# Kernel tuning notes

Hardware: AMD Instinct MI355X
Metric: run time of the kernel (lower is better)

The kernel has to match this reference:

```python
import jax, jax.numpy as jnp
import numpy as np
from jax import lax

MAX_DEPTH = 8
NLEAVES = 2 ** MAX_DEPTH      # 256
NNODES = 2 ** MAX_DEPTH - 1   # 255 (preorder-numbered inner nodes)
NCLASS = 10
EPS = 1e-5
BATCH = 8192


def _build_paths():
    # Reproduce the torch preorder node numbering and DFS leaf numbering.
    node_ctr = [0]
    leaf_paths = []
    def rec(depth, path):
        idx = node_ctr[0]; node_ctr[0] += 1
        if depth < MAX_DEPTH:
            rec(depth + 1, path + [(idx, 0)])   # left child: prob (1 - p)
            rec(depth + 1, path + [(idx, 1)])   # right child: prob p
        else:
            leaf_paths.append(path + [(idx, 0)])
            leaf_paths.append(path + [(idx, 1)])
    rec(1, [])
    nidx = np.array([[n for n, _ in p] for p in leaf_paths], dtype=np.int32)  # [L, D]
    dirs = np.array([[d for _, d in p] for p in leaf_paths], dtype=bool)      # [L, D]
    return nidx, dirs

NODE_IDX, DIRS = _build_paths()


def _bn(x, g, b):
    # training-mode batchnorm over all dims except channel axis 1 (biased var)
    axes = tuple(i for i in range(x.ndim) if i != 1)
    m = x.mean(axes, keepdims=True)
    v = x.var(axes, keepdims=True)
    shape = [1] * x.ndim; shape[1] = -1
    return (x - m) * lax.rsqrt(v + EPS) * g.reshape(shape) + b.reshape(shape)


def _conv(x, w, b):
    y = lax.conv_general_dilated(x, w, (1, 1), 'VALID',
                                 dimension_numbers=('NCHW', 'OIHW', 'NCHW'))
    return y + b[None, :, None, None]


def _pool2(x):
    return lax.reduce_window(x, -jnp.inf, lax.max, (1, 1, 2, 2), (1, 1, 2, 2), 'VALID')


def setup_inputs() -> dict:
    ks = jax.random.split(jax.random.key(0), 12)
    f32 = jnp.float32
    return {
        'x': jax.random.normal(ks[0], (BATCH, 1, 28, 28), f32),
        'y': jax.random.randint(ks[1], (BATCH,), 0, NCLASS),
        'conv1_w': 0.1 * jax.random.normal(ks[2], (20, 1, 5, 5), f32),
        'conv1_b': jnp.zeros((20,), f32),
        'conv2_w': 0.05 * jax.random.normal(ks[3], (50, 20, 5, 5), f32),
        'conv2_b': jnp.zeros((50,), f32),
        'g1': jnp.ones((20,), f32), 'be1': jnp.zeros((20,), f32),
        'g2': jnp.ones((50,), f32), 'be2': jnp.zeros((50,), f32),
        'fc1_w': 0.05 * jax.random.normal(ks[4], (10, 800), f32),
        'fc1_b': jnp.zeros((10,), f32),
        'g3': jnp.ones((10,), f32), 'be3': jnp.zeros((10,), f32),
        'theta_w': 0.3 * jax.random.normal(ks[5], (NNODES, 10), f32),
        'theta_b': jnp.zeros((NNODES,), f32),
        'pi': jax.random.uniform(ks[6], (NLEAVES, NCLASS), f32, 0.1, 1.0),
    }


def reference(x, y, conv1_w, conv1_b, conv2_w, conv2_b, g1, be1, g2, be2,
              fc1_w, fc1_b, g3, be3, theta_w, theta_b, pi):
    B = x.shape[0]
    # CNN backbone
    h = _pool2(jax.nn.relu(_bn(_conv(x, conv1_w, conv1_b), g1, be1)))
    h = _pool2(jax.nn.relu(_bn(_conv(h, conv2_w, conv2_b), g2, be2)))
    h = h.reshape(B, 4 * 4 * 50)
    h = jax.nn.relu(_bn(h @ fc1_w.T + fc1_b, g3, be3))        # [B, 10]
    # batched soft-tree gating: one fused GEMM for all 255 tiny Linear(10,1)
    p = jax.nn.sigmoid(h @ theta_w.T + theta_b)                # [B, NNODES]
    g = p[:, NODE_IDX]                                         # [B, L, D]
    mu = jnp.prod(jnp.where(DIRS[None], g, 1.0 - g), axis=2)   # [B, L]
    # pi is a row-stochastic distribution (uniform at torch init)
    pi_n = pi / pi.sum(1, keepdims=True)
    # stale P from __init__: uniform mu (1/L) @ pi  ->  column means of pi
    P_prev = jnp.broadcast_to(pi_n.mean(0), (B, NCLASS))       # [B, C]
    # vectorized cal_pi (soft-EM update of leaf distributions)
    Y = jax.nn.one_hot(y, NCLASS, dtype=mu.dtype)              # [B, C]
    S = mu.T @ (Y / P_prev)                                    # [L, C]
    pi_h = pi_n * S
    pi_new = pi_h / pi_h.sum(1, keepdims=True)
    # cal_P and log
    P = mu @ pi_new                                            # [B, C]
    return jnp.log(P)
```

## Files before the change

kernel.cpp:

```cpp
#include <hip/hip_runtime.h>
#include <hip/hip_bf16.h>
#include <math.h>

typedef __attribute__((ext_vector_type(8))) short short8v;
typedef __attribute__((ext_vector_type(4))) float float4v;

static const size_t F_RAWP1B = 0;
static const size_t F_C2P    = 14155776;
static const size_t F_PART1  = 20709376;
static const size_t F_PART2  = 21037056;
static const size_t F_PART3  = 21241856;
static const size_t F_BN1    = 21246976;
static const size_t F_BN2    = 21247016;
static const size_t F_BN3    = 21247116;
static const size_t F_SRAW   = 21247136;
static const size_t F_PINEW  = 21249696;
static const size_t F_WB2    = 21252256;
static const size_t F_WB1    = 21271712;
static const size_t F_SPART  = 21272224;
static const size_t F_HRAW   = 0;
static const size_t F_MU     = 81920;

__device__ __forceinline__ float relu_(float v) { return v > 0.f ? v : 0.f; }

__device__ __forceinline__ unsigned int pack_bf16x2(float a, float b) {
  __hip_bfloat16 ha = __float2bfloat16(a), hb = __float2bfloat16(b);
  unsigned short ua, ub;
  __builtin_memcpy(&ua, &ha, 2); __builtin_memcpy(&ub, &hb, 2);
  return ((unsigned int)ub << 16) | ua;
}

__device__ __forceinline__ float pick_(float a, float b, bool mx) {
  return mx ? fmaxf(a, b) : fminf(a, b);
}

__global__ __launch_bounds__(256) void k_wprep1(
    const float* __restrict__ w, unsigned short* __restrict__ wb1)
{
  const int i = blockIdx.x * 256 + threadIdx.x;
  const int n = i >> 5, k = i & 31;
  const int kh = k / 6, kw = k - kh*6;
  float v = (n < 20 && kh < 5 && kw < 5) ? w[n*25 + kh*5 + kw] : 0.f;
  __hip_bfloat16 h = __float2bfloat16(v);
  unsigned short u; __builtin_memcpy(&u, &h, 2);
  wb1[i] = u;
}

__global__ __launch_bounds__(256) void k_wprep2(
    const float* __restrict__ w, unsigned short* __restrict__ wb)
{
  const int idx = blockIdx.x * 256 + threadIdx.x;
  const int cc = idx >> 9;
  const int rem = idx & 511;
  const int n = rem >> 3, j = rem & 7;
  float v = 0.f;
  if (cc < 75 && n < 50) {
    const int khw = cc / 3, icg = cc - khw*3;
    const int ic = icg*8 + j;
    if (ic < 20) {
      const int kh = khw / 5, kw = khw - kh*5;
      v = w[((n*20 + ic)*5 + kh)*5 + kw];
    }
  }
  __hip_bfloat16 h = __float2bfloat16(v);
  unsigned short u; __builtin_memcpy(&u, &h, 2);
  wb[idx] = u;
}

__global__ __launch_bounds__(256) void k_conv1_mfma(
    const float* __restrict__ x, const unsigned short* __restrict__ wb1,
    const float* __restrict__ g1, unsigned int* __restrict__ rawp1b,
    float* __restrict__ part)
{
  __shared__ alignas(16) unsigned short xpk[1568];
  __shared__ float sred[4][32], qred[4][32];
  const int tid = threadIdx.x, img = blockIdx.x;
  const float* xp = x + (size_t)img * 784;
  for (int i = tid; i < 784; i += 256) {
    const int r = i / 28, c = i - r*28;
    __hip_bfloat16 h = __float2bfloat16(xp[i]);
    unsigned short u; __builtin_memcpy(&u, &h, 2);
    xpk[r*28 + c] = u;
    if (c >= 1) xpk[784 + r*28 + (c-1)] = u;
    else        xpk[784 + r*28 + 27]  = 0;
  }
  __syncthreads();
  const int wave = tid >> 6, lane = tid & 63, lo = lane & 15, hi = lane >> 4;

  const short8v bfr0 = *(const short8v*)(wb1 + (lo*32 + hi*8));
  const short8v bfr1 = *(const short8v*)(wb1 + ((16+lo)*32 + hi*8));

  const unsigned enc = (hi==0) ? 0x0E020100u
                     : (hi==1) ? 0x1D1C100Fu
                     : (hi==2) ? 0x2C2B2A1Eu
                     :           0x003A3938u;
  const int off0 = enc & 255, off1 = (enc>>8)&255, off2 = (enc>>16)&255, off3 = enc>>24;
  const unsigned int* xpd = (const unsigned int*)xpk;
  const int pb   = (lo & 1) * 392;
  const int oyp  = (lo >> 1) & 1, qoff = lo >> 2;
  const int inv  = pb + (6*wave + oyp)*14;

  float4v acc[9][2];
  #pragma unroll
  for (int t = 0; t < 9; ++t) {
    acc[t][0] = (float4v){0.f,0.f,0.f,0.f};
    acc[t][1] = (float4v){0.f,0.f,0.f,0.f};
  }

  #pragma unroll
  for (int tt = 0; tt < 9; ++tt) {
    const int pylc = (tt*4) / 12;
    const int pxlc = (tt*4) - pylc*12;
    const int base = inv + pylc*28 + pxlc + qoff;
    union { unsigned int u[4]; short8v v; } cu;
    cu.u[0] = xpd[base + off0];
    cu.u[1] = xpd[base + off1];
    cu.u[2] = xpd[base + off2];
    cu.u[3] = xpd[base + off3];
    acc[tt][0] = __builtin_amdgcn_mfma_f32_16x16x32_bf16(cu.v, bfr0, acc[tt][0], 0, 0, 0);
    acc[tt][1] = __builtin_amdgcn_mfma_f32_16x16x32_bf16(cu.v, bfr1, acc[tt][1], 0, 0, 0);
  }

  const bool gp0 = (g1[lo] >= 0.f);
  const bool gp1 = (lo < 4) ? (g1[16+lo] >= 0.f) : true;
  float sv0 = 0.f, qv0 = 0.f, sv1 = 0.f, qv1 = 0.f;
  unsigned int* dst = rawp1b + (size_t)img * 1728;
  #pragma unroll
  for (int tt = 0; tt < 9; ++tt) {
    const int T = wave*9 + tt;
    const int q = T*4 + hi;
    const float4v v0 = acc[tt][0];
    const float4v v1 = acc[tt][1];
    #pragma unroll
    for (int r = 0; r < 4; ++r) { sv0 += v0[r]; qv0 += v0[r]*v0[r]; }
    #pragma unroll
    for (int r = 0; r < 4; ++r) { sv1 += v1[r]; qv1 += v1[r]*v1[r]; }
    const float p0 = pick_(pick_(v0[0], v0[1], gp0), pick_(v0[2], v0[3], gp0), gp0);
    const float p1 = pick_(pick_(v1[0], v1[1], gp1), pick_(v1[2], v1[3], gp1), gp1);
    const float o0 = __shfl_down(p0, 1);
    const float o1 = __shfl_down(p1, 1);
    if ((lo & 1) == 0) {
      dst[q*12 + (lo >> 1)] = pack_bf16x2(p0, o0);
      if (lo < 8)
        dst[q*12 + 8 + (lo >> 1)] = pack_bf16x2(p1, o1);
    }
  }
  sv0 += __shfl_down(sv0, 32); qv0 += __shfl_down(qv0, 32);
  sv0 += __shfl_down(sv0, 16); qv0 += __shfl_down(qv0, 16);
  sv1 += __shfl_down(sv1, 32); qv1 += __shfl_down(qv1, 32);
  sv1 += __shfl_down(sv1, 16); qv1 += __shfl_down(qv1, 16);
  if (hi == 0) {
    sred[wave][lo] = sv0; sred[wave][16+lo] = sv1;
    qred[wave][lo] = qv0; qred[wave][16+lo] = qv1;
  }
  __syncthreads();
  if (tid < 20) {
    float s = 0.f, q = 0.f;
    #pragma unroll
    for (int w2 = 0; w2 < 4; ++w2) { s += sred[w2][tid]; q += qred[w2][tid]; }
    part[(size_t)img*40 + tid]      = s;
    part[(size_t)img*40 + 20 + tid] = q;
  }
}

__global__ __launch_bounds__(256) void k_conv2_mfma(
    const unsigned int* __restrict__ rawp1b, const unsigned short* __restrict__ wb,
    const float* __restrict__ bn1, const float* __restrict__ g2,
    float* __restrict__ c2p, float* __restrict__ part)
{
  __shared__ alignas(16) unsigned int in4[6912];
  __shared__ float sred[4][64], qred[4][64];
  __shared__ alignas(16) float bn1i[48];
  __shared__ unsigned short aofft[76];
  const int tid = threadIdx.x, blk = blockIdx.x;
  if (tid < 24) {
    const float sc = (tid < 20) ? bn1[tid]      : 0.f;
    const float sh = (tid < 20) ? bn1[20 + tid] : 0.f;
    bn1i[2*tid] = sc; bn1i[2*tid + 1] = sh;
  }
  if (tid < 76) {
    const int cc2 = tid > 74 ? 74 : tid;
    const int khw = cc2 / 3, icg = cc2 - khw*3;
    const int kh = khw / 5, kw = khw - kh*5;
    aofft[tid] = (unsigned short)((kh*12 + kw)*48 + icg*16);
  }
  __syncthreads();

  const uint4* src4 = (const uint4*)(rawp1b + (size_t)blk * 6912);
  uint4* dst4 = (uint4*)in4;
  int jj = tid % 3;
  for (int k = 0; k < 7; ++k) {
    const int i = k*256 + tid;
    if (i < 1728) {
      const uint4 v = src4[i];
      unsigned int o[4];
      #pragma unroll
      for (int m = 0; m < 4; ++m) {
        const float4 ss = *(const float4*)(bn1i + jj*16 + m*4);
        const unsigned int u = (m==0) ? v.x : (m==1) ? v.y : (m==2) ? v.z : v.w;
        const float a = __uint_as_float(u << 16);
        const float b = __uint_as_float(u & 0xffff0000u);
        const float ra = relu_(fmaf(a, ss.x, ss.y));
        const float rb = relu_(fmaf(b, ss.z, ss.w));
        o[m] = pack_bf16x2(ra, rb);
      }
      uint4 ov; ov.x = o[0]; ov.y = o[1]; ov.z = o[2]; ov.w = o[3];
      dst4[i] = ov;
    }
    jj = (jj == 2) ? 0 : jj + 1;
  }
  __syncthreads();

  const int wave = tid >> 6, lane = tid & 63;
  const int lo = lane & 15, hi = lane >> 4;
  const char* ibase = (const char*)in4 + wave * 6912;

  const char* bA[4];
  #pragma unroll
  for (int a = 0; a < 4; ++a) {
    const int m = a*16 + lo;
    bA[a] = ibase + ((m >> 3) * 12 + (m & 7)) * 48;
  }
  unsigned short aoffs[19];
  #pragma unroll
  for (int s = 0; s < 19; ++s) aoffs[s] = aofft[s*4 + hi];
  const unsigned short* wbase = wb + hi*512 + lo*8;

  bool gpos[4];
  #pragma unroll
  for (int nf = 0; nf < 4; ++nf) {
    const int n = nf*16 + lo;
    gpos[nf] = (n < 50) ? (g2[n] >= 0.f) : true;
  }

  float4v acc[4][4];
  #pragma unroll
  for (int a = 0; a < 4; ++a)
    #pragma unroll
    for (int nf = 0; nf < 4; ++nf) acc[a][nf] = (float4v){0.f, 0.f, 0.f, 0.f};

  #pragma unroll
  for (int s = 0; s < 19; ++s) {
    short8v av[4], bv[4];
    #pragma unroll
    for (int am = 0; am < 4; ++am)
      av[am] = *(const short8v*)(bA[am] + aoffs[s]);
    const unsigned short* wrow = wbase + s*2048;
    #pragma unroll
    for (int nf = 0; nf < 4; ++nf)
      bv[nf] = *(const short8v*)(wrow + nf*128);
    #pragma unroll
    for (int am = 0; am < 4; ++am)
      #pragma unroll
      for (int nf = 0; nf < 4; ++nf)
        acc[am][nf] = __builtin_amdgcn_mfma_f32_16x16x32_bf16(av[am], bv[nf], acc[am][nf], 0, 0, 0);
  }

  const int img = blk*4 + wave;
  #pragma unroll
  for (int nf = 0; nf < 4; ++nf) {
    const int n = nf*16 + lo;
    float sv = 0.f, qv = 0.f;
    #pragma unroll
    for (int am = 0; am < 4; ++am) {
      float4v v = acc[am][nf];
      #pragma unroll
      for (int r = 0; r < 4; ++r) { sv += v[r]; qv += v[r]*v[r]; }
      float h0 = gpos[nf] ? fmaxf(v[0], v[1]) : fminf(v[0], v[1]);
      float h1 = gpos[nf] ? fmaxf(v[2], v[3]) : fminf(v[2], v[3]);
      const float o0 = __shfl_xor(h0, 32);
      const float o1 = __shfl_xor(h1, 32);
      h0 = gpos[nf] ? fmaxf(h0, o0) : fminf(h0, o0);
      h1 = gpos[nf] ? fmaxf(h1, o1) : fminf(h1, o1);
      if (hi < 2 && n < 50) {
        float2 o; o.x = h0; o.y = h1;
        *(float2*)(c2p + (size_t)img*800 + n*16 + am*4 + hi*2) = o;
      }
    }
    sv += __shfl_down(sv, 32); qv += __shfl_down(qv, 32);
    sv += __shfl_down(sv, 16); qv += __shfl_down(qv, 16);
    if (hi == 0) { sred[wave][nf*16 + lo] = sv; qred[wave][nf*16 + lo] = qv; }
  }
  __syncthreads();
  if (tid < 100) {
    const int ch = tid < 50 ? tid : tid - 50;
    float t = 0.f;
    if (tid < 50) {
      #pragma unroll
      for (int w2 = 0; w2 < 4; ++w2) t += sred[w2][ch];
      part[(size_t)blk*100 + ch] = t;
    } else {
      #pragma unroll
      for (int w2 = 0; w2 < 4; ++w2) t += qred[w2][ch];
      part[(size_t)blk*100 + 50 + ch] = t;
    }
  }
}

__global__ __launch_bounds__(256) void k_bn_fin(
    const float* __restrict__ part, int nblk, int nch, float N,
    const float* __restrict__ g, const float* __restrict__ b,
    float* __restrict__ out)
{
  __shared__ double rd[4][2];
  const int tid = threadIdx.x, ch = blockIdx.x;
  const int lane = tid & 63, wid = tid >> 6;
  double s = 0.0, q = 0.0;
  for (int i = tid; i < nblk; i += 256) {
    s += (double)part[(size_t)i*2*nch + ch];
    q += (double)part[(size_t)i*2*nch + nch + ch];
  }
  #pragma unroll
  for (int off = 32; off > 0; off >>= 1) { s += __shfl_down(s, off); q += __shfl_down(q, off); }
  if (lane == 0) { rd[wid][0] = s; rd[wid][1] = q; }
  __syncthreads();
  if (tid == 0) {
    double S = rd[0][0] + rd[1][0] + rd[2][0] + rd[3][0];
    double Q = rd[0][1] + rd[1][1] + rd[2][1] + rd[3][1];
    double mean = S / (double)N;
    double var  = Q / (double)N - mean * mean;
    if (var < 0.0) var = 0.0;
    float scv = (float)((double)g[ch] / sqrt(var + 1e-5));
    out[ch]       = scv;
    out[nch + ch] = b[ch] - (float)mean * scv;
  }
}

__global__ __launch_bounds__(256) void k_fc1(
    const float* __restrict__ c2p, const float* __restrict__ bn2,
    const float* __restrict__ fw, float* __restrict__ h_raw,
    float* __restrict__ part)
{
  __shared__ alignas(16) float wl[8000];
  __shared__ float s2[50], h2[50];
  __shared__ float red[4][20];
  const int tid = threadIdx.x;
  for (int i = tid; i < 2000; i += 256)
    ((float4*)wl)[i] = ((const float4*)fw)[i];
  if (tid < 50) { s2[tid] = bn2[tid]; h2[tid] = bn2[50 + tid]; }
  __syncthreads();
  const int s = tid >> 3, kc = tid & 7;
  const int sample = blockIdx.x * 32 + s;
  const float* xr = c2p + (size_t)sample * 800 + kc * 100;
  float acc[10];
  #pragma unroll
  for (int f = 0; f < 10; ++f) acc[f] = 0.f;
  #pragma unroll 5
  for (int c = 0; c < 25; ++c) {
    const int k = kc*100 + c*4;
    float4 v = *(const float4*)(xr + c*4);
    const int oc = k >> 4;
    const float sc = s2[oc], sh = h2[oc];
    v.x = relu_(v.x*sc + sh); v.y = relu_(v.y*sc + sh);
    v.z = relu_(v.z*sc + sh); v.w = relu_(v.w*sc + sh);
    #pragma unroll
    for (int f = 0; f < 10; ++f) {
      const float4 wv = *(const float4*)(wl + f*800 + k);
      acc[f] += v.x*wv.x + v.y*wv.y + v.z*wv.z + v.w*wv.w;
    }
  }
  const int lane = tid & 63, wid = tid >> 6;
  #pragma unroll
  for (int f = 0; f < 10; ++f) {
    acc[f] += __shfl_down(acc[f], 4);
    acc[f] += __shfl_down(acc[f], 2);
    acc[f] += __shfl_down(acc[f], 1);
    float a2 = (kc == 0) ? acc[f] : 0.f;
    float q2 = (kc == 0) ? acc[f]*acc[f] : 0.f;
    if (kc == 0) h_raw[(size_t)sample*10 + f] = acc[f];
    a2 += __shfl_down(a2, 32); q2 += __shfl_down(q2, 32);
    a2 += __shfl_down(a2, 16); q2 += __shfl_down(q2, 16);
    a2 += __shfl_down(a2, 8);  q2 += __shfl_down(q2, 8);
    if (lane == 0) { red[wid][f] = a2; red[wid][10+f] = q2; }
  }
  __syncthreads();
  if (tid < 20) {
    float t = 0.f;
    #pragma unroll
    for (int w2 = 0; w2 < 4; ++w2) t += red[w2][tid];
    part[(size_t)blockIdx.x*20 + tid] = t;
  }
}

__global__ __launch_bounds__(256) void k_theta_mu(
    const float* __restrict__ h_raw, const float* __restrict__ bn3,
    const float* __restrict__ tw, const float* __restrict__ tb,
    float* __restrict__ mu)
{
  __shared__ float twt[10][256];
  __shared__ float tbl[256];
  __shared__ float hl[32][10];
  __shared__ float pl[32][256];
  const int tid = threadIdx.x, blk = blockIdx.x;
  for (int i = tid; i < 2550; i += 256) {
    const int node = i / 10, f = i - node*10;
    twt[f][node] = tw[i];
  }
  if (tid < 10) twt[tid][255] = 0.f;
  tbl[tid] = (tid < 255) ? tb[tid] : 0.f;
  for (int i = tid; i < 320; i += 256) {
    const int ss = i / 10, f = i - ss*10;
    hl[ss][f] = relu_(h_raw[(size_t)blk*320 + i] * bn3[f] + bn3[10 + f]);
  }
  __syncthreads();
  const int node = tid;
  for (int i2 = 0; i2 < 32; ++i2) {
    float h[10];
    #pragma unroll
    for (int f = 0; f < 10; ++f) h[f] = hl[i2][f];
    float d = tbl[node];
    #pragma unroll
    for (int f = 0; f < 10; ++f) d += h[f] * twt[f][node];
    pl[i2][node] = (node < 255) ? 1.f / (1.f + __expf(-d)) : 0.f;
  }
  __syncthreads();
  for (int i2 = 0; i2 < 32; ++i2) {
    float m = 1.f; int idx = 0;
    #pragma unroll
    for (int k = 0; k < 8; ++k) {
      const int dir = (tid >> (7 - k)) & 1;
      const float pv = pl[i2][idx];
      m *= dir ? pv : (1.f - pv);
      idx += dir ? (1 << (7 - k)) : 1;
    }
    mu[(size_t)(blk*32 + i2)*256 + tid] = m;
  }
}

__global__ __launch_bounds__(256) void k_S_part(
    const float* __restrict__ mu, const int* __restrict__ y,
    float* __restrict__ spart)
{
  const int tid = threadIdx.x;
  const int b0 = blockIdx.x * 32;
  float acc[10];
  #pragma unroll
  for (int c = 0; c < 10; ++c) acc[c] = 0.f;
  for (int s = 0; s < 32; ++s) {
    const int b = b0 + s;
    const float m = mu[(size_t)b*256 + tid];
    const int c = y[b];
    #pragma unroll
    for (int cc = 0; cc < 10; ++cc) acc[cc] += (c == cc) ? m : 0.f;
  }
  float* dst = spart + (size_t)blockIdx.x*2560 + tid*10;
  #pragma unroll
  for (int cc = 0; cc < 10; ++cc) dst[cc] = acc[cc];
}

__global__ __launch_bounds__(256) void k_S_red(
    const float* __restrict__ spart, float* __restrict__ S)
{
  const int e = blockIdx.x * 256 + threadIdx.x;
  float s = 0.f;
  for (int k = 0; k < 256; ++k) s += spart[(size_t)k*2560 + e];
  S[e] = s;
}

__global__ __launch_bounds__(256) void k_pi(
    const float* __restrict__ pi, const float* __restrict__ S,
    float* __restrict__ pi_new)
{
  __shared__ float pin[2560];
  __shared__ float Pp[10];
  const int t = threadIdx.x;
  float row[10]; float rs = 0.f;
  #pragma unroll
  for (int c = 0; c < 10; ++c) { row[c] = pi[t*10 + c]; rs += row[c]; }
  #pragma unroll
  for (int c = 0; c < 10; ++c) { row[c] /= rs; pin[t*10 + c] = row[c]; }
  __syncthreads();
  if (t < 10) {
    float s = 0.f;
    for (int l = 0; l < 256; ++l) s += pin[l*10 + t];
    Pp[t] = s / 256.f;
  }
  __syncthreads();
  float hs = 0.f; float ph[10];
  #pragma unroll
  for (int c = 0; c < 10; ++c) {
    const float Sv = S[t*10 + c] / Pp[c];
    ph[c] = row[c] * Sv;
    hs += ph[c];
  }
  #pragma unroll
  for (int c = 0; c < 10; ++c) pi_new[t*10 + c] = ph[c] / hs;
}

__global__ __launch_bounds__(256) void k_out(
    const float* __restrict__ mu, const float* __restrict__ pn,
    float* __restrict__ out)
{
  __shared__ float plt[10][260];
  const int tid = threadIdx.x;
  if (tid < 256) {
    #pragma unroll
    for (int c = 0; c < 10; ++c) plt[c][tid] = pn[tid*10 + c];
  }
  __syncthreads();
  const int gid = blockIdx.x * 256 + tid;
  const int b = gid / 10, c = gid % 10;
  const float4* mr4 = (const float4*)(mu + (size_t)b * 256);
  const float*  pc  = &plt[c][0];
  float a0 = 0.f, a1 = 0.f;
  #pragma unroll 4
  for (int l4 = 0; l4 < 64; ++l4) {
    const float4 m = mr4[l4];
    const float4 p = *(const float4*)(pc + 4*l4);
    a0 += m.x*p.x + m.y*p.y;
    a1 += m.z*p.z + m.w*p.w;
  }
  out[gid] = logf(a0 + a1);
}

extern "C" void kernel_launch(void* const* d_in, const int* in_sizes, int n_in,
                              void* d_out, int out_size, void* d_ws, size_t ws_size,
                              hipStream_t stream)
{
  const float* x   = (const float*)d_in[0];
  const int*   y   = (const int*)  d_in[1];
  const float* c1w = (const float*)d_in[2];
  const float* c2w = (const float*)d_in[4];
  const float* g1  = (const float*)d_in[6];
  const float* be1 = (const float*)d_in[7];
  const float* g2  = (const float*)d_in[8];
  const float* be2 = (const float*)d_in[9];
  const float* fw  = (const float*)d_in[10];
  const float* g3  = (const float*)d_in[12];
  const float* be3 = (const float*)d_in[13];
  const float* thw = (const float*)d_in[14];
  const float* thb = (const float*)d_in[15];
  const float* pi  = (const float*)d_in[16];
  float* ws  = (float*)d_ws;
  float* out = (float*)d_out;

  unsigned int*   rawp1b = (unsigned int*)(ws + F_RAWP1B);
  float*          c2p    = ws + F_C2P;
  float*          part1  = ws + F_PART1;
  float*          part2  = ws + F_PART2;
  float*          part3  = ws + F_PART3;
  float*          bn1    = ws + F_BN1;
  float*          bn2    = ws + F_BN2;
  float*          bn3    = ws + F_BN3;
  float*          sraw   = ws + F_SRAW;
  float*          pinew  = ws + F_PINEW;
  unsigned short* wb2    = (unsigned short*)(ws + F_WB2);
  unsigned short* wb1    = (unsigned short*)(ws + F_WB1);
  float*          spart  = ws + F_SPART;
  float*          hraw   = ws + F_HRAW;
  float*          muB    = ws + F_MU;

  k_wprep1<<<4, 256, 0, stream>>>(c1w, wb1);
  k_wprep2<<<152, 256, 0, stream>>>(c2w, wb2);
  k_conv1_mfma<<<8192, 256, 0, stream>>>(x, wb1, g1, rawp1b, part1);
  k_bn_fin<<<20, 256, 0, stream>>>(part1, 8192, 20, 8192.f * 576.f, g1, be1, bn1);
  k_conv2_mfma<<<2048, 256, 0, stream>>>(rawp1b, wb2, bn1, g2, c2p, part2);
  k_bn_fin<<<50, 256, 0, stream>>>(part2, 2048, 50, 8192.f * 64.f, g2, be2, bn2);
  k_fc1<<<256, 256, 0, stream>>>(c2p, bn2, fw, hraw, part3);
  k_bn_fin<<<10, 256, 0, stream>>>(part3, 256, 10, 8192.f, g3, be3, bn3);
  k_theta_mu<<<256, 256, 0, stream>>>(hraw, bn3, thw, thb, muB);
  k_S_part<<<256, 256, 0, stream>>>(muB, y, spart);
  k_S_red<<<10, 256, 0, stream>>>(spart, sraw);
  k_pi<<<1, 256, 0, stream>>>(pi, sraw, pinew);
  k_out<<<320, 256, 0, stream>>>(muB, pinew, out);
}
```

Baseline: 187.4 us.

## Process multiple images per block with register-staged prefetch in conv1 and conv2

conv1 now handles four images per block and conv2 two image groups per block. In both, the next image's global load goes into registers while the current one is computed on MFMA, with double-buffered LDS in conv1. This hides global load latency behind MFMA work and amortises the per-block weight and setup loads. The cost is a quarter and a half as many blocks, extra register pressure from the staging buffers (which may lower occupancy), and an added barrier per iteration.

```diff
diff --git a/kernel.cpp b/kernel.cpp
--- a/kernel.cpp
+++ b/kernel.cpp
@@ -30,6 +30,12 @@
   return ((unsigned int)ub << 16) | ua;
 }
 
+__device__ __forceinline__ unsigned short cvt_bf16(float a) {
+  __hip_bfloat16 h = __float2bfloat16(a);
+  unsigned short u; __builtin_memcpy(&u, &h, 2);
+  return u;
+}
+
 __device__ __forceinline__ float pick_(float a, float b, bool mx) {
   return mx ? fmaxf(a, b) : fminf(a, b);
 }
@@ -41,9 +47,7 @@
   const int n = i >> 5, k = i & 31;
   const int kh = k / 6, kw = k - kh*6;
   float v = (n < 20 && kh < 5 && kw < 5) ? w[n*25 + kh*5 + kw] : 0.f;
-  __hip_bfloat16 h = __float2bfloat16(v);
-  unsigned short u; __builtin_memcpy(&u, &h, 2);
-  wb1[i] = u;
+  wb1[i] = cvt_bf16(v);
 }
 
 __global__ __launch_bounds__(256) void k_wprep2(
@@ -62,9 +66,7 @@
       v = w[((n*20 + ic)*5 + kh)*5 + kw];
     }
   }
-  __hip_bfloat16 h = __float2bfloat16(v);
-  unsigned short u; __builtin_memcpy(&u, &h, 2);
-  wb[idx] = u;
+  wb[idx] = cvt_bf16(v);
 }
 
 __global__ __launch_bounds__(256) void k_conv1_mfma(
@@ -72,94 +74,134 @@
     const float* __restrict__ g1, unsigned int* __restrict__ rawp1b,
     float* __restrict__ part)
 {
-  __shared__ alignas(16) unsigned short xpk[1568];
+  __shared__ alignas(16) unsigned short xpk[2][1568];
   __shared__ float sred[4][32], qred[4][32];
-  const int tid = threadIdx.x, img = blockIdx.x;
-  const float* xp = x + (size_t)img * 784;
-  for (int i = tid; i < 784; i += 256) {
-    const int r = i / 28, c = i - r*28;
-    __hip_bfloat16 h = __float2bfloat16(xp[i]);
-    unsigned short u; __builtin_memcpy(&u, &h, 2);
-    xpk[r*28 + c] = u;
-    if (c >= 1) xpk[784 + r*28 + (c-1)] = u;
-    else        xpk[784 + r*28 + 27]  = 0;
-  }
-  __syncthreads();
+  const int tid = threadIdx.x, blk = blockIdx.x;
+  const int img0 = blk * 4;
   const int wave = tid >> 6, lane = tid & 63, lo = lane & 15, hi = lane >> 4;
 
   const short8v bfr0 = *(const short8v*)(wb1 + (lo*32 + hi*8));
   const short8v bfr1 = *(const short8v*)(wb1 + ((16+lo)*32 + hi*8));
-
   const unsigned enc = (hi==0) ? 0x0E020100u
                      : (hi==1) ? 0x1D1C100Fu
                      : (hi==2) ? 0x2C2B2A1Eu
                      :           0x003A3938u;
   const int off0 = enc & 255, off1 = (enc>>8)&255, off2 = (enc>>16)&255, off3 = enc>>24;
-  const unsigned int* xpd = (const unsigned int*)xpk;
   const int pb   = (lo & 1) * 392;
   const int oyp  = (lo >> 1) & 1, qoff = lo >> 2;
   const int inv  = pb + (6*wave + oyp)*14;
-
-  float4v acc[9][2];
-  #pragma unroll
-  for (int t = 0; t < 9; ++t) {
-    acc[t][0] = (float4v){0.f,0.f,0.f,0.f};
-    acc[t][1] = (float4v){0.f,0.f,0.f,0.f};
-  }
-
-  #pragma unroll
-  for (int tt = 0; tt < 9; ++tt) {
-    const int pylc = (tt*4) / 12;
-    const int pxlc = (tt*4) - pylc*12;
-    const int base = inv + pylc*28 + pxlc + qoff;
-    union { unsigned int u[4]; short8v v; } cu;
-    cu.u[0] = xpd[base + off0];
-    cu.u[1] = xpd[base + off1];
-    cu.u[2] = xpd[base + off2];
-    cu.u[3] = xpd[base + off3];
-    acc[tt][0] = __builtin_amdgcn_mfma_f32_16x16x32_bf16(cu.v, bfr0, acc[tt][0], 0, 0, 0);
-    acc[tt][1] = __builtin_amdgcn_mfma_f32_16x16x32_bf16(cu.v, bfr1, acc[tt][1], 0, 0, 0);
-  }
-
   const bool gp0 = (g1[lo] >= 0.f);
   const bool gp1 = (lo < 4) ? (g1[16+lo] >= 0.f) : true;
-  float sv0 = 0.f, qv0 = 0.f, sv1 = 0.f, qv1 = 0.f;
-  unsigned int* dst = rawp1b + (size_t)img * 1728;
-  #pragma unroll
-  for (int tt = 0; tt < 9; ++tt) {
-    const int T = wave*9 + tt;
-    const int q = T*4 + hi;
-    const float4v v0 = acc[tt][0];
-    const float4v v1 = acc[tt][1];
-    #pragma unroll
-    for (int r = 0; r < 4; ++r) { sv0 += v0[r]; qv0 += v0[r]*v0[r]; }
-    #pragma unroll
-    for (int r = 0; r < 4; ++r) { sv1 += v1[r]; qv1 += v1[r]*v1[r]; }
-    const float p0 = pick_(pick_(v0[0], v0[1], gp0), pick_(v0[2], v0[3], gp0), gp0);
-    const float p1 = pick_(pick_(v1[0], v1[1], gp1), pick_(v1[2], v1[3], gp1), gp1);
-    const float o0 = __shfl_down(p0, 1);
-    const float o1 = __shfl_down(p1, 1);
-    if ((lo & 1) == 0) {
-      dst[q*12 + (lo >> 1)] = pack_bf16x2(p0, o0);
-      if (lo < 8)
-        dst[q*12 + 8 + (lo >> 1)] = pack_bf16x2(p1, o1);
-    }
-  }
-  sv0 += __shfl_down(sv0, 32); qv0 += __shfl_down(qv0, 32);
-  sv0 += __shfl_down(sv0, 16); qv0 += __shfl_down(qv0, 16);
-  sv1 += __shfl_down(sv1, 32); qv1 += __shfl_down(qv1, 32);
-  sv1 += __shfl_down(sv1, 16); qv1 += __shfl_down(qv1, 16);
-  if (hi == 0) {
-    sred[wave][lo] = sv0; sred[wave][16+lo] = sv1;
-    qred[wave][lo] = qv0; qred[wave][16+lo] = qv1;
-  }
-  __syncthreads();
-  if (tid < 20) {
-    float s = 0.f, q = 0.f;
-    #pragma unroll
-    for (int w2 = 0; w2 < 4; ++w2) { s += sred[w2][tid]; q += qred[w2][tid]; }
-    part[(size_t)img*40 + tid]      = s;
-    part[(size_t)img*40 + 20 + tid] = q;
+  const int r0 = tid / 28,        c0 = tid - r0*28;
+  const int r1 = (tid+256) / 28,  c1 = (tid+256) - r1*28;
+  const int r2 = (tid+512) / 28,  c2 = (tid+512) - r2*28;
+  const int r3 = (tid+768) / 28,  c3 = (tid+768) - r3*28;
+
+  float st0, st1, st2, st3;
+  {
+    const float* xp = x + (size_t)img0 * 784;
+    st0 = xp[tid]; st1 = xp[tid+256]; st2 = xp[tid+512];
+    st3 = (tid < 16) ? xp[tid+768] : 0.f;
+  }
+  {
+    unsigned short* b0 = &xpk[0][0];
+    const unsigned short u0 = cvt_bf16(st0), u1 = cvt_bf16(st1), u2 = cvt_bf16(st2);
+    b0[r0*28 + c0] = u0;
+    if (c0 >= 1) b0[784 + r0*28 + c0 - 1] = u0; else b0[784 + r0*28 + 27] = 0;
+    b0[r1*28 + c1] = u1;
+    if (c1 >= 1) b0[784 + r1*28 + c1 - 1] = u1; else b0[784 + r1*28 + 27] = 0;
+    b0[r2*28 + c2] = u2;
+    if (c2 >= 1) b0[784 + r2*28 + c2 - 1] = u2; else b0[784 + r2*28 + 27] = 0;
+    if (tid < 16) {
+      const unsigned short u3 = cvt_bf16(st3);
+      b0[r3*28 + c3] = u3;
+      if (c3 >= 1) b0[784 + r3*28 + c3 - 1] = u3;
+    }
+  }
+  __syncthreads();
+
+  int cur = 0;
+  for (int ii = 0; ii < 4; ++ii) {
+    if (ii < 3) {
+      const float* xp = x + (size_t)(img0 + ii + 1) * 784;
+      st0 = xp[tid]; st1 = xp[tid+256]; st2 = xp[tid+512];
+      st3 = (tid < 16) ? xp[tid+768] : 0.f;
+    }
+    const unsigned int* xpd = (const unsigned int*)&xpk[cur][0];
+    float4v acc[9][2];
+    #pragma unroll
+    for (int t = 0; t < 9; ++t) {
+      acc[t][0] = (float4v){0.f,0.f,0.f,0.f};
+      acc[t][1] = (float4v){0.f,0.f,0.f,0.f};
+    }
+    #pragma unroll
+    for (int tt = 0; tt < 9; ++tt) {
+      const int pylc = (tt*4) / 12;
+      const int pxlc = (tt*4) - pylc*12;
+      const int base = inv + pylc*28 + pxlc + qoff;
+      union { unsigned int u[4]; short8v v; } cu;
+      cu.u[0] = xpd[base + off0];
+      cu.u[1] = xpd[base + off1];
+      cu.u[2] = xpd[base + off2];
+      cu.u[3] = xpd[base + off3];
+      acc[tt][0] = __builtin_amdgcn_mfma_f32_16x16x32_bf16(cu.v, bfr0, acc[tt][0], 0, 0, 0);
+      acc[tt][1] = __builtin_amdgcn_mfma_f32_16x16x32_bf16(cu.v, bfr1, acc[tt][1], 0, 0, 0);
+    }
+    float sv0 = 0.f, qv0 = 0.f, sv1 = 0.f, qv1 = 0.f;
+    unsigned int* dst = rawp1b + (size_t)(img0 + ii) * 1728;
+    #pragma unroll
+    for (int tt = 0; tt < 9; ++tt) {
+      const int T = wave*9 + tt;
+      const int q = T*4 + hi;
+      const float4v v0 = acc[tt][0];
+      const float4v v1 = acc[tt][1];
+      #pragma unroll
+      for (int r = 0; r < 4; ++r) { sv0 += v0[r]; qv0 += v0[r]*v0[r]; }
+      #pragma unroll
+      for (int r = 0; r < 4; ++r) { sv1 += v1[r]; qv1 += v1[r]*v1[r]; }
+      const float p0 = pick_(pick_(v0[0], v0[1], gp0), pick_(v0[2], v0[3], gp0), gp0);
+      const float p1 = pick_(pick_(v1[0], v1[1], gp1), pick_(v1[2], v1[3], gp1), gp1);
+      const float o0 = __shfl_down(p0, 1);
+      const float o1 = __shfl_down(p1, 1);
+      if ((lo & 1) == 0) {
+        dst[q*12 + (lo >> 1)] = pack_bf16x2(p0, o0);
+        if (lo < 8)
+          dst[q*12 + 8 + (lo >> 1)] = pack_bf16x2(p1, o1);
+      }
+    }
+    sv0 += __shfl_down(sv0, 32); qv0 += __shfl_down(qv0, 32);
+    sv0 += __shfl_down(sv0, 16); qv0 += __shfl_down(qv0, 16);
+    sv1 += __shfl_down(sv1, 32); qv1 += __shfl_down(qv1, 32);
+    sv1 += __shfl_down(sv1, 16); qv1 += __shfl_down(qv1, 16);
+    if (hi == 0) {
+      sred[wave][lo] = sv0; sred[wave][16+lo] = sv1;
+      qred[wave][lo] = qv0; qred[wave][16+lo] = qv1;
+    }
+    __syncthreads();
+    if (tid < 20) {
+      float s = 0.f, q = 0.f;
+      #pragma unroll
+      for (int w2 = 0; w2 < 4; ++w2) { s += sred[w2][tid]; q += qred[w2][tid]; }
+      part[(size_t)(img0 + ii)*40 + tid]      = s;
+      part[(size_t)(img0 + ii)*40 + 20 + tid] = q;
+    }
+    if (ii < 3) {
+      unsigned short* bn = &xpk[cur ^ 1][0];
+      const unsigned short u0 = cvt_bf16(st0), u1 = cvt_bf16(st1), u2 = cvt_bf16(st2);
+      bn[r0*28 + c0] = u0;
+      if (c0 >= 1) bn[784 + r0*28 + c0 - 1] = u0; else bn[784 + r0*28 + 27] = 0;
+      bn[r1*28 + c1] = u1;
+      if (c1 >= 1) bn[784 + r1*28 + c1 - 1] = u1; else bn[784 + r1*28 + 27] = 0;
+      bn[r2*28 + c2] = u2;
+      if (c2 >= 1) bn[784 + r2*28 + c2 - 1] = u2; else bn[784 + r2*28 + 27] = 0;
+      if (tid < 16) {
+        const unsigned short u3 = cvt_bf16(st3);
+        bn[r3*28 + c3] = u3;
+        if (c3 >= 1) bn[784 + r3*28 + c3 - 1] = u3;
+      }
+    }
+    __syncthreads();
+    cur ^= 1;
   }
 }
 
@@ -184,36 +226,22 @@
     const int kh = khw / 5, kw = khw - kh*5;
     aofft[tid] = (unsigned short)((kh*12 + kw)*48 + icg*16);
   }
-  __syncthreads();
-
-  const uint4* src4 = (const uint4*)(rawp1b + (size_t)blk * 6912);
-  uint4* dst4 = (uint4*)in4;
-  int jj = tid % 3;
-  for (int k = 0; k < 7; ++k) {
-    const int i = k*256 + tid;
-    if (i < 1728) {
-      const uint4 v = src4[i];
-      unsigned int o[4];
-      #pragma unroll
-      for (int m = 0; m < 4; ++m) {
-        const float4 ss = *(const float4*)(bn1i + jj*16 + m*4);
-        const unsigned int u = (m==0) ? v.x : (m==1) ? v.y : (m==2) ? v.z : v.w;
-        const float a = __uint_as_float(u << 16);
-        const float b = __uint_as_float(u & 0xffff0000u);
-        const float ra = relu_(fmaf(a, ss.x, ss.y));
-        const float rb = relu_(fmaf(b, ss.z, ss.w));
-        o[m] = pack_bf16x2(ra, rb);
-      }
-      uint4 ov; ov.x = o[0]; ov.y = o[1]; ov.z = o[2]; ov.w = o[3];
-      dst4[i] = ov;
-    }
-    jj = (jj == 2) ? 0 : jj + 1;
-  }
-  __syncthreads();
 
   const int wave = tid >> 6, lane = tid & 63;
   const int lo = lane & 15, hi = lane >> 4;
   const char* ibase = (const char*)in4 + wave * 6912;
+  const int jj0 = tid % 3;
+
+  uint4 stg[7];
+  {
+    const uint4* src4 = (const uint4*)(rawp1b + (size_t)(blk*2) * 6912);
+    #pragma unroll
+    for (int k = 0; k < 7; ++k) {
+      const int i = k*256 + tid;
+      if (i < 1728) stg[k] = src4[i];
+    }
+  }
+  __syncthreads();
 
   const char* bA[4];
   #pragma unroll
@@ -225,7 +253,6 @@
   #pragma unroll
   for (int s = 0; s < 19; ++s) aoffs[s] = aofft[s*4 + hi];
   const unsigned short* wbase = wb + hi*512 + lo*8;
-
   bool gpos[4];
   #pragma unroll
   for (int nf = 0; nf < 4; ++nf) {
@@ -233,66 +260,104 @@
     gpos[nf] = (n < 50) ? (g2[n] >= 0.f) : true;
   }
 
-  float4v acc[4][4];
-  #pragma unroll
-  for (int a = 0; a < 4; ++a)
-    #pragma unroll
-    for (int nf = 0; nf < 4; ++nf) acc[a][nf] = (float4v){0.f, 0.f, 0.f, 0.f};
-
-  #pragma unroll
-  for (int s = 0; s < 19; ++s) {
-    short8v av[4], bv[4];
-    #pragma unroll
-    for (int am = 0; am < 4; ++am)
-      av[am] = *(const short8v*)(bA[am] + aoffs[s]);
-    const unsigned short* wrow = wbase + s*2048;
-    #pragma unroll
-    for (int nf = 0; nf < 4; ++nf)
-      bv[nf] = *(const short8v*)(wrow + nf*128);
-    #pragma unroll
-    for (int am = 0; am < 4; ++am)
+  for (int g = 0; g < 2; ++g) {
+    {
+      uint4* dst4 = (uint4*)in4;
+      int jj = jj0;
+      #pragma unroll
+      for (int k = 0; k < 7; ++k) {
+        const int i = k*256 + tid;
+        if (i < 1728) {
+          const uint4 v = stg[k];
+          unsigned int o[4];
+          #pragma unroll
+          for (int m = 0; m < 4; ++m) {
+            const float4 ss = *(const float4*)(bn1i + jj*16 + m*4);
+            const unsigned int u = (m==0) ? v.x : (m==1) ? v.y : (m==2) ? v.z : v.w;
+            const float a = __uint_as_float(u << 16);
+            const float b = __uint_as_float(u & 0xffff0000u);
+            const float ra = relu_(fmaf(a, ss.x, ss.y));
+            const float rb = relu_(fmaf(b, ss.z, ss.w));
+            o[m] = pack_bf16x2(ra, rb);
+          }
+          uint4 ov; ov.x = o[0]; ov.y = o[1]; ov.z = o[2]; ov.w = o[3];
+          dst4[i] = ov;
+        }
+        jj = (jj == 2) ? 0 : jj + 1;
+      }
+    }
+    __syncthreads();
+    if (g == 0) {
+      const uint4* src4 = (const uint4*)(rawp1b + (size_t)(blk*2 + 1) * 6912);
+      #pragma unroll
+      for (int k = 0; k < 7; ++k) {
+        const int i = k*256 + tid;
+        if (i < 1728) stg[k] = src4[i];
+      }
+    }
+
+    float4v acc[4][4];
+    #pragma unroll
+    for (int a = 0; a < 4; ++a)
+      #pragma unroll
+      for (int nf = 0; nf < 4; ++nf) acc[a][nf] = (float4v){0.f, 0.f, 0.f, 0.f};
+
+    #pragma unroll
+    for (int s = 0; s < 19; ++s) {
+      short8v av[4], bv[4];
+      #pragma unroll
+      for (int am = 0; am < 4; ++am)
+        av[am] = *(const short8v*)(bA[am] + aoffs[s]);
+      const unsigned short* wrow = wbase + s*2048;
       #pragma unroll
       for (int nf = 0; nf < 4; ++nf)
-        acc[am][nf] = __builtin_amdgcn_mfma_f32_16x16x32_bf16(av[am], bv[nf], acc[am][nf], 0, 0, 0);
-  }
-
-  const int img = blk*4 + wave;
-  #pragma unroll
-  for (int nf = 0; nf < 4; ++nf) {
-    const int n = nf*16 + lo;
-    float sv = 0.f, qv = 0.f;
-    #pragma unroll
-    for (int am = 0; am < 4; ++am) {
-      float4v v = acc[am][nf];
-      #pragma unroll
-      for (int r = 0; r < 4; ++r) { sv += v[r]; qv += v[r]*v[r]; }
-      float h0 = gpos[nf] ? fmaxf(v[0], v[1]) : fminf(v[0], v[1]);
-      float h1 = gpos[nf] ? fmaxf(v[2], v[3]) : fminf(v[2], v[3]);
-      const float o0 = __shfl_xor(h0, 32);
-      const float o1 = __shfl_xor(h1, 32);
-      h0 = gpos[nf] ? fmaxf(h0, o0) : fminf(h0, o0);
-      h1 = gpos[nf] ? fmaxf(h1, o1) : fminf(h1, o1);
-      if (hi < 2 && n < 50) {
-        float2 o; o.x = h0; o.y = h1;
-        *(float2*)(c2p + (size_t)img*800 + n*16 + am*4 + hi*2) = o;
+        bv[nf] = *(const short8v*)(wrow + nf*128);
+      #pragma unroll
+      for (int am = 0; am < 4; ++am)
+        #pragma unroll
+        for (int nf = 0; nf < 4; ++nf)
+          acc[am][nf] = __builtin_amdgcn_mfma_f32_16x16x32_bf16(av[am], bv[nf], acc[am][nf], 0, 0, 0);
+    }
+
+    const int gidx = blk*2 + g;
+    const int img = gidx*4 + wave;
+    #pragma unroll
+    for (int nf = 0; nf < 4; ++nf) {
+      const int n = nf*16 + lo;
+      float sv = 0.f, qv = 0.f;
+      #pragma unroll
+      for (int am = 0; am < 4; ++am) {
+        float4v v = acc[am][nf];
+        #pragma unroll
+        for (int r = 0; r < 4; ++r) { sv += v[r]; qv += v[r]*v[r]; }
+        float h0 = gpos[nf] ? fmaxf(v[0], v[1]) : fminf(v[0], v[1]);
+        float h1 = gpos[nf] ? fmaxf(v[2], v[3]) : fminf(v[2], v[3]);
+        const float o0 = __shfl_xor(h0, 32);
+        const float o1 = __shfl_xor(h1, 32);
+        h0 = gpos[nf] ? fmaxf(h0, o0) : fminf(h0, o0);
+        h1 = gpos[nf] ? fmaxf(h1, o1) : fminf(h1, o1);
+        if (hi < 2 && n < 50) {
+          float2 o; o.x = h0; o.y = h1;
+          *(float2*)(c2p + (size_t)img*800 + n*16 + am*4 + hi*2) = o;
+        }
       }
-    }
-    sv += __shfl_down(sv, 32); qv += __shfl_down(qv, 32);
-    sv += __shfl_down(sv, 16); qv += __shfl_down(qv, 16);
-    if (hi == 0) { sred[wave][nf*16 + lo] = sv; qred[wave][nf*16 + lo] = qv; }
-  }
-  __syncthreads();
-  if (tid < 100) {
-    const int ch = tid < 50 ? tid : tid - 50;
-    float t = 0.f;
-    if (tid < 50) {
-      #pragma unroll
-      for (int w2 = 0; w2 < 4; ++w2) t += sred[w2][ch];
-      part[(size_t)blk*100 + ch] = t;
-    } else {
-      #pragma unroll
-      for (int w2 = 0; w2 < 4; ++w2) t += qred[w2][ch];
-      part[(size_t)blk*100 + 50 + ch] = t;
+      sv += __shfl_down(sv, 32); qv += __shfl_down(qv, 32);
+      sv += __shfl_down(sv, 16); qv += __shfl_down(qv, 16);
+      if (hi == 0) { sred[wave][nf*16 + lo] = sv; qred[wave][nf*16 + lo] = qv; }
+    }
+    __syncthreads();
+    if (tid < 100) {
+      const int ch = tid < 50 ? tid : tid - 50;
+      float t = 0.f;
+      if (tid < 50) {
+        #pragma unroll
+        for (int w2 = 0; w2 < 4; ++w2) t += sred[w2][ch];
+        part[(size_t)gidx*100 + ch] = t;
+      } else {
+        #pragma unroll
+        for (int w2 = 0; w2 < 4; ++w2) t += qred[w2][ch];
+        part[(size_t)gidx*100 + 50 + ch] = t;
+      }
     }
   }
 }
@@ -552,9 +617,9 @@
 
   k_wprep1<<<4, 256, 0, stream>>>(c1w, wb1);
   k_wprep2<<<152, 256, 0, stream>>>(c2w, wb2);
-  k_conv1_mfma<<<8192, 256, 0, stream>>>(x, wb1, g1, rawp1b, part1);
+  k_conv1_mfma<<<2048, 256, 0, stream>>>(x, wb1, g1, rawp1b, part1);
   k_bn_fin<<<20, 256, 0, stream>>>(part1, 8192, 20, 8192.f * 576.f, g1, be1, bn1);
-  k_conv2_mfma<<<2048, 256, 0, stream>>>(rawp1b, wb2, bn1, g2, c2p, part2);
+  k_conv2_mfma<<<1024, 256, 0, stream>>>(rawp1b, wb2, bn1, g2, c2p, part2);
   k_bn_fin<<<50, 256, 0, stream>>>(part2, 2048, 50, 8192.f * 64.f, g2, be2, bn2);
   k_fc1<<<256, 256, 0, stream>>>(c2p, bn2, fw, hraw, part3);
   k_bn_fin<<<10, 256, 0, stream>>>(part3, 256, 10, 8192.f, g3, be3, bn3);
```

Result: slower. 215.1 us (+14.8%).
